# Kernel tuning notes

Hardware: AMD Instinct MI355X
Metric: run time of the kernel (lower is better)

The kernel has to match this reference:

```python
import jax, jax.numpy as jnp
import numpy as np

B, C, H, W = 8, 256, 128, 128
NW = 512  # n_weights (depthwise multiplier 2)
EPS = 1e-5
SPARSITY = 0.5


def setup_inputs() -> dict:
    key = jax.random.key(0)
    k_x, k_sign, k_mask, k_w1 = jax.random.split(key, 4)
    x = jax.random.normal(k_x, (B, C, H, W), dtype=jnp.float32)
    gamma = jnp.ones((C,), dtype=jnp.float32)
    beta = jnp.zeros((C,), dtype=jnp.float32)
    # frozen binary/sparse LBP depthwise weights in {-1, 0, +1}
    sign = jax.random.bernoulli(k_sign, 0.5, (NW, 1, 3, 3)).astype(jnp.float32) * 2.0 - 1.0
    inactive = jax.random.uniform(k_mask, (NW, 1, 3, 3)) > SPARSITY
    lbp_w = jnp.where(inactive, 0.0, sign)
    # 1x1 conv params (PyTorch default init scale)
    bound = 1.0 / np.sqrt(NW)
    w1 = jax.random.uniform(k_w1, (C, NW, 1, 1), minval=-bound, maxval=bound, dtype=jnp.float32)
    b1 = jnp.zeros((C,), dtype=jnp.float32)
    return {"x": x, "gamma": gamma, "beta": beta, "lbp_w": lbp_w, "w1": w1, "b1": b1}


def reference(x, gamma, beta, lbp_w, w1, b1):
    # BatchNorm2d in training mode: biased batch stats over (N, H, W)
    mean = jnp.mean(x, axis=(0, 2, 3), keepdims=True)
    var = jnp.var(x, axis=(0, 2, 3), keepdims=True)
    xn = (x - mean) * jax.lax.rsqrt(var + EPS)
    xn = xn * gamma[None, :, None, None] + beta[None, :, None, None]
    # depthwise 3x3 conv, padding=1, groups=C (depth multiplier NW//C)
    y = jax.lax.conv_general_dilated(
        xn, lbp_w, window_strides=(1, 1), padding=((1, 1), (1, 1)),
        dimension_numbers=("NCHW", "OIHW", "NCHW"), feature_group_count=C)
    y = jax.nn.relu(y)
    # 1x1 conv NW -> C plus bias, then residual add
    z = jax.lax.conv_general_dilated(
        y, w1, window_strides=(1, 1), padding=((0, 0), (0, 0)),
        dimension_numbers=("NCHW", "OIHW", "NCHW"))
    z = z + b1[None, :, None, None]
    return z + x
```

## Files before the change

### kernel.cpp

```cpp
#include <hip/hip_runtime.h>

#define B_ 8
#define C_ 256
#define H_ 128
#define W_ 128
#define NW_ 512
#define HW_ (H_*W_)
#define EPS_ 1e-5f

typedef __attribute__((ext_vector_type(8))) short bf16x8;
typedef __attribute__((ext_vector_type(4))) float f32x4;

__device__ __forceinline__ unsigned short f2bf(float f) {
  unsigned u = __float_as_uint(f);
  u += 0x7fffu + ((u >> 16) & 1u);
  return (unsigned short)(u >> 16);
}
__device__ __forceinline__ float bf2f(unsigned short h) {
  return __uint_as_float(((unsigned)h) << 16);
}
__device__ __forceinline__ float bflo(unsigned u) { return __uint_as_float(u << 16); }
__device__ __forceinline__ float bfhi(unsigned u) { return __uint_as_float(u & 0xffff0000u); }

__global__ __launch_bounds__(256)
void bn_partial(const float* __restrict__ x, float* __restrict__ psum,
                float* __restrict__ psq) {
  const int b = blockIdx.x, c = blockIdx.y, tid = threadIdx.x;
  const float4* p = (const float4*)(x + (size_t)(b*C_ + c) * HW_);
  float s = 0.f, s2 = 0.f;
  #pragma unroll
  for (int i = 0; i < 16; ++i) {
    float4 v = p[tid + i*256];
    s  += v.x + v.y + v.z + v.w;
    s2 += v.x*v.x + v.y*v.y + v.z*v.z + v.w*v.w;
  }
  #pragma unroll
  for (int off = 32; off > 0; off >>= 1) {
    s  += __shfl_down(s, off);
    s2 += __shfl_down(s2, off);
  }
  __shared__ float rs[4], rq[4];
  if ((tid & 63) == 0) { rs[tid >> 6] = s; rq[tid >> 6] = s2; }
  __syncthreads();
  if (tid == 0) {
    float S = rs[0]+rs[1]+rs[2]+rs[3], S2 = rq[0]+rq[1]+rq[2]+rq[3];
    psum[c*B_ + b] = S;
    psq [c*B_ + b] = S2;
  }
}

__global__ __launch_bounds__(256)
void bn_final(float* __restrict__ wsf, const float* __restrict__ gamma,
              const float* __restrict__ beta) {
  const int c = threadIdx.x;
  float S = 0.f, S2 = 0.f;
  #pragma unroll
  for (int b = 0; b < B_; ++b) { S += wsf[512 + c*B_ + b]; S2 += wsf[2560 + c*B_ + b]; }
  const float n = (float)(B_*HW_);
  float mean = S / n;
  float var  = S2 / n - mean*mean;
  float scl  = gamma[c] * rsqrtf(var + EPS_);
  wsf[c]       = scl;
  wsf[C_ + c]  = beta[c] - mean*scl;
}

__global__ __launch_bounds__(64)
void w1prep(const float* __restrict__ w1, ushort* __restrict__ w1f) {
  const int l15 = threadIdx.x & 15, quad = threadIdx.x >> 4;
  const int mtG = blockIdx.x >> 4, ks = blockIdx.x & 15;
  const float* src = w1 + (size_t)(mtG*16 + l15)*NW_ + ks*32 + quad*8;
  float4 f0 = *(const float4*)src, f1 = *(const float4*)(src + 4);
  union { unsigned u[4]; uint4 q; } cv;
  cv.u[0] = (unsigned)f2bf(f0.x) | ((unsigned)f2bf(f0.y) << 16);
  cv.u[1] = (unsigned)f2bf(f0.z) | ((unsigned)f2bf(f0.w) << 16);
  cv.u[2] = (unsigned)f2bf(f1.x) | ((unsigned)f2bf(f1.y) << 16);
  cv.u[3] = (unsigned)f2bf(f1.z) | ((unsigned)f2bf(f1.w) << 16);
  ((uint4*)w1f)[blockIdx.x*64 + threadIdx.x] = cv.q;
}

template<bool PREW1>
__global__ __launch_bounds__(256, 4)
void fused_mfma(const float* __restrict__ x, const float* __restrict__ lbpw,
                const float* __restrict__ w1raw, const ushort* __restrict__ w1f,
                const float* __restrict__ b1, const float* __restrict__ sc_sh,
                float* __restrict__ out) {
  const int tid  = threadIdx.x;
  const int b    = blockIdx.z;
  const int h0   = blockIdx.y * 4;
  const int w0   = blockIdx.x * 16;
  const int wave = tid >> 6;
  const int lane = tid & 63;
  const int l15  = lane & 15;
  const int quad = lane >> 4;
  const int cl   = tid >> 4;
  const int jj   = tid & 15;

  __shared__ float  s_scale[C_];
  __shared__ float  s_shift[C_];
  __shared__ float  s_b1[C_];
  __shared__ __align__(16) float  s_xn[2][16][6][20];
  __shared__ __align__(16) ushort s_yT[2][64][40];
  __shared__ __align__(16) ushort s_wc[2][32][16];

  s_scale[tid] = sc_sh[tid];
  s_shift[tid] = sc_sh[C_ + tid];
  s_b1[tid]    = b1[tid];

  int geo[7];
  unsigned actmask = 0, padmask = 0;
  #pragma unroll
  for (int k = 0; k < 7; ++k) {
    geo[k] = 0;
    const int e = jj + 16*k;
    if (e < 108) {
      const int r   = e / 18;
      const int col = e - r*18;
      const int lofs = cl*120 + r*20 + col;
      const int h = h0 + r - 1;
      const int w = w0 + col - 1;
      if (h >= 0 && h < H_ && w >= 0 && w < W_) {
        actmask |= (1u << k);
        geo[k] = ((cl*HW_ + h*W_ + w) << 11) | lofs;
      } else {
        padmask |= (1u << k);
        geo[k] = lofs;
      }
    }
  }
  {
    float* p0 = &s_xn[0][0][0][0];
    float* p1 = &s_xn[1][0][0][0];
    #pragma unroll
    for (int k = 0; k < 7; ++k)
      if (padmask & (1u << k)) { p0[geo[k] & 2047] = 0.f; p1[geo[k] & 2047] = 0.f; }
  }
  const int woA = tid / 9,         wjA = tid - woA*9;
  const int woB = (tid + 256) / 9, wjB = (tid + 256) - woB*9;

  f32x4 acc[4][4];
  #pragma unroll
  for (int mt = 0; mt < 4; ++mt)
    #pragma unroll
    for (int nt = 0; nt < 4; ++nt) { f32x4 z = {0.f,0.f,0.f,0.f}; acc[mt][nt] = z; }

  __syncthreads();

  {
    const float scl = s_scale[cl];
    const float sh  = s_shift[cl];
    const float* xc = x + (size_t)(b*C_) * HW_;
    float* xb = &s_xn[0][0][0][0];
    #pragma unroll
    for (int k = 0; k < 7; ++k)
      if (actmask & (1u << k)) xb[geo[k] & 2047] = fmaf(xc[geo[k] >> 11], scl, sh);
    s_wc[0][woA][wjA] = f2bf(lbpw[woA*9 + wjA]);
    if (tid < 32) s_wc[0][woB][wjB] = f2bf(lbpw[woB*9 + wjB]);
  }
  __syncthreads();

  #pragma unroll 2
  for (int kc = 0; kc < 16; ++kc) {
    const int p = kc & 1;

    {
      float v[6][3];
      #pragma unroll
      for (int rr = 0; rr < 6; ++rr)
        #pragma unroll
        for (int dj = 0; dj < 3; ++dj)
          v[rr][dj] = s_xn[p][cl][rr][jj + dj];

      const uint4 qa = *(const uint4*)&s_wc[p][2*cl][0];
      const uint4 qb = *(const uint4*)&s_wc[p][2*cl + 1][0];
      const float wA[9] = { bflo(qa.x), bfhi(qa.x), bflo(qa.y), bfhi(qa.y),
                            bflo(qa.z), bfhi(qa.z), bflo(qa.w), bfhi(qa.w),
                            bf2f(s_wc[p][2*cl][8]) };
      const float wB[9] = { bflo(qb.x), bfhi(qb.x), bflo(qb.y), bfhi(qb.y),
                            bflo(qb.z), bfhi(qb.z), bflo(qb.w), bfhi(qb.w),
                            bf2f(s_wc[p][2*cl + 1][8]) };
      float a0[4] = {0.f,0.f,0.f,0.f}, a1[4] = {0.f,0.f,0.f,0.f};
      #pragma unroll
      for (int r = 0; r < 4; ++r)
        #pragma unroll
        for (int di = 0; di < 3; ++di)
          #pragma unroll
          for (int dj = 0; dj < 3; ++dj) {
            const float t = v[r + di][dj];
            a0[r] = fmaf(wA[di*3 + dj], t, a0[r]);
            a1[r] = fmaf(wB[di*3 + dj], t, a1[r]);
          }
      #pragma unroll
      for (int r = 0; r < 4; ++r) {
        const unsigned pk = (unsigned)f2bf(fmaxf(a0[r], 0.f)) |
                            ((unsigned)f2bf(fmaxf(a1[r], 0.f)) << 16);
        *(unsigned*)&s_yT[p][r*16 + jj][2*cl] = pk;
      }
    }

    if (kc < 15) {
      const int c0 = (kc + 1) * 16;
      const float scl = s_scale[c0 + cl];
      const float sh  = s_shift[c0 + cl];
      const float* xc = x + (size_t)(b*C_ + c0) * HW_;
      float* xb = &s_xn[p ^ 1][0][0][0];
      #pragma unroll
      for (int k = 0; k < 7; ++k)
        if (actmask & (1u << k)) xb[geo[k] & 2047] = fmaf(xc[geo[k] >> 11], scl, sh);
      const int o0 = (kc + 1) * 32;
      s_wc[p ^ 1][woA][wjA] = f2bf(lbpw[(o0 + woA)*9 + wjA]);
      if (tid < 32) s_wc[p ^ 1][woB][wjB] = f2bf(lbpw[(o0 + woB)*9 + wjB]);
    }

    __syncthreads();

    bf16x8 bfr[4];
    #pragma unroll
    for (int nt = 0; nt < 4; ++nt)
      bfr[nt] = *(const bf16x8*)&s_yT[p][nt*16 + l15][quad*8];

    #pragma unroll
    for (int mt = 0; mt < 4; ++mt) {
      bf16x8 afr;
      if constexpr (PREW1) {
        union { uint4 q; bf16x8 v; } cv;
        cv.q = *(const uint4*)(w1f + (size_t)(((wave*4 + mt)*16 + kc)*64 + lane)*8);
        afr = cv.v;
      } else {
        const float* wp = w1raw + (size_t)(wave*64 + mt*16 + l15)*NW_ + kc*32 + quad*8;
        const float4 f0 = *(const float4*)wp;
        const float4 f1 = *(const float4*)(wp + 4);
        union { unsigned u[4]; bf16x8 v; } cv;
        cv.u[0] = (unsigned)f2bf(f0.x) | ((unsigned)f2bf(f0.y) << 16);
        cv.u[1] = (unsigned)f2bf(f0.z) | ((unsigned)f2bf(f0.w) << 16);
        cv.u[2] = (unsigned)f2bf(f1.x) | ((unsigned)f2bf(f1.y) << 16);
        cv.u[3] = (unsigned)f2bf(f1.z) | ((unsigned)f2bf(f1.w) << 16);
        afr = cv.v;
      }
      #pragma unroll
      for (int nt = 0; nt < 4; ++nt)
        acc[mt][nt] = __builtin_amdgcn_mfma_f32_16x16x32_bf16(afr, bfr[nt], acc[mt][nt], 0, 0, 0);
    }
  }

  #pragma unroll
  for (int mt = 0; mt < 4; ++mt) {
    #pragma unroll
    for (int nt = 0; nt < 4; ++nt) {
      const int h = h0 + nt;
      #pragma unroll
      for (int i = 0; i < 4; ++i) {
        const int ch = wave*64 + mt*16 + quad*4 + i;
        const size_t o = ((size_t)(b*C_ + ch)*H_ + h)*W_ + (w0 + l15);
        out[o] = acc[mt][nt][i] + s_b1[ch] + x[o];
      }
    }
  }
}

extern "C" void kernel_launch(void* const* d_in, const int* in_sizes, int n_in,
                              void* d_out, int out_size, void* d_ws, size_t ws_size,
                              hipStream_t stream) {
  const float* x     = (const float*)d_in[0];
  const float* gamma = (const float*)d_in[1];
  const float* beta  = (const float*)d_in[2];
  const float* lbpw  = (const float*)d_in[3];
  const float* w1    = (const float*)d_in[4];
  const float* b1    = (const float*)d_in[5];
  float* out = (float*)d_out;

  float* wsf = (float*)d_ws;
  ushort* w1f = (ushort*)((char*)d_ws + 18432);
  const bool pre = ws_size >= (size_t)(18432 + 262144);

  bn_partial<<<dim3(B_, C_), 256, 0, stream>>>(x, wsf + 512, wsf + 2560);
  bn_final<<<1, 256, 0, stream>>>(wsf, gamma, beta);

  dim3 grid(W_/16, H_/4, B_);
  if (pre) {
    w1prep<<<256, 64, 0, stream>>>(w1, w1f);
    fused_mfma<true><<<grid, 256, 0, stream>>>(x, lbpw, w1, w1f, b1, wsf, out);
  } else {
    fused_mfma<false><<<grid, 256, 0, stream>>>(x, lbpw, w1, w1f, b1, wsf, out);
  }
}
```

Measured before the change: 415.9 us.

## Prefetch next-next channel chunk into registers to overlap global loads

Global loads of x and the LBP weights for chunk kc+2 are now issued into registers one iteration early. The stores into the LDS double buffer then use values already resident in registers, so global-memory latency overlaps with the depthwise and MFMA work instead of stalling before the barrier. The depthwise loop is also restructured to stream one row at a time from LDS rather than holding a 6x3 window. The cost is higher register pressure from the seven prefetch registers plus two weight registers, which could reduce occupancy.

```diff
diff --git a/kernel.cpp b/kernel.cpp
--- a/kernel.cpp
+++ b/kernel.cpp
@@ -145,6 +145,9 @@
 
   __syncthreads();
 
+  float reg[7];
+  float wreg0 = 0.f, wreg1 = 0.f;
+
   {
     const float scl = s_scale[cl];
     const float sh  = s_shift[cl];
@@ -155,6 +158,12 @@
       if (actmask & (1u << k)) xb[geo[k] & 2047] = fmaf(xc[geo[k] >> 11], scl, sh);
     s_wc[0][woA][wjA] = f2bf(lbpw[woA*9 + wjA]);
     if (tid < 32) s_wc[0][woB][wjB] = f2bf(lbpw[woB*9 + wjB]);
+    const float* xc1 = xc + (size_t)16 * HW_;
+    #pragma unroll
+    for (int k = 0; k < 7; ++k)
+      if (actmask & (1u << k)) reg[k] = xc1[geo[k] >> 11];
+    wreg0 = lbpw[(32 + woA)*9 + wjA];
+    if (tid < 32) wreg1 = lbpw[(32 + woB)*9 + wjB];
   }
   __syncthreads();
 
@@ -163,13 +172,6 @@
     const int p = kc & 1;
 
     {
-      float v[6][3];
-      #pragma unroll
-      for (int rr = 0; rr < 6; ++rr)
-        #pragma unroll
-        for (int dj = 0; dj < 3; ++dj)
-          v[rr][dj] = s_xn[p][cl][rr][jj + dj];
-
       const uint4 qa = *(const uint4*)&s_wc[p][2*cl][0];
       const uint4 qb = *(const uint4*)&s_wc[p][2*cl + 1][0];
       const float wA[9] = { bflo(qa.x), bfhi(qa.x), bflo(qa.y), bfhi(qa.y),
@@ -180,15 +182,19 @@
                             bf2f(s_wc[p][2*cl + 1][8]) };
       float a0[4] = {0.f,0.f,0.f,0.f}, a1[4] = {0.f,0.f,0.f,0.f};
       #pragma unroll
-      for (int r = 0; r < 4; ++r)
+      for (int rr = 0; rr < 6; ++rr) {
+        const float v0 = s_xn[p][cl][rr][jj];
+        const float v1 = s_xn[p][cl][rr][jj + 1];
+        const float v2 = s_xn[p][cl][rr][jj + 2];
         #pragma unroll
-        for (int di = 0; di < 3; ++di)
-          #pragma unroll
-          for (int dj = 0; dj < 3; ++dj) {
-            const float t = v[r + di][dj];
-            a0[r] = fmaf(wA[di*3 + dj], t, a0[r]);
-            a1[r] = fmaf(wB[di*3 + dj], t, a1[r]);
+        for (int r = 0; r < 4; ++r) {
+          const int di = rr - r;
+          if (di >= 0 && di < 3) {
+            a0[r] = fmaf(wA[di*3+2], v2, fmaf(wA[di*3+1], v1, fmaf(wA[di*3+0], v0, a0[r])));
+            a1[r] = fmaf(wB[di*3+2], v2, fmaf(wB[di*3+1], v1, fmaf(wB[di*3+0], v0, a1[r])));
           }
+        }
+      }
       #pragma unroll
       for (int r = 0; r < 4; ++r) {
         const unsigned pk = (unsigned)f2bf(fmaxf(a0[r], 0.f)) |
@@ -198,17 +204,25 @@
     }
 
     if (kc < 15) {
-      const int c0 = (kc + 1) * 16;
-      const float scl = s_scale[c0 + cl];
-      const float sh  = s_shift[c0 + cl];
-      const float* xc = x + (size_t)(b*C_ + c0) * HW_;
+      const int c1 = (kc + 1) * 16;
+      const float scl = s_scale[c1 + cl];
+      const float sh  = s_shift[c1 + cl];
       float* xb = &s_xn[p ^ 1][0][0][0];
       #pragma unroll
       for (int k = 0; k < 7; ++k)
-        if (actmask & (1u << k)) xb[geo[k] & 2047] = fmaf(xc[geo[k] >> 11], scl, sh);
-      const int o0 = (kc + 1) * 32;
-      s_wc[p ^ 1][woA][wjA] = f2bf(lbpw[(o0 + woA)*9 + wjA]);
-      if (tid < 32) s_wc[p ^ 1][woB][wjB] = f2bf(lbpw[(o0 + woB)*9 + wjB]);
+        if (actmask & (1u << k)) xb[geo[k] & 2047] = fmaf(reg[k], scl, sh);
+      s_wc[p ^ 1][woA][wjA] = f2bf(wreg0);
+      if (tid < 32) s_wc[p ^ 1][woB][wjB] = f2bf(wreg1);
+    }
+
+    if (kc < 14) {
+      const float* xc = x + (size_t)(b*C_ + (kc + 2)*16) * HW_;
+      #pragma unroll
+      for (int k = 0; k < 7; ++k)
+        if (actmask & (1u << k)) reg[k] = xc[geo[k] >> 11];
+      const int o2 = (kc + 2) * 32;
+      wreg0 = lbpw[(o2 + woA)*9 + wjA];
+      if (tid < 32) wreg1 = lbpw[(o2 + woB)*9 + wjB];
     }
 
     __syncthreads();
```

Measured after the change: 488.1 us. 1.17x slower.
